# Optimization experiments

Hardware: AMD Instinct MI355X
Metric: run time of the kernel (lower is better)

Reference implementation:

```python
import jax, jax.numpy as jnp
import numpy as np

T, S, B, D, H, DH, DI = 1024, 1024, 4, 1024, 16, 64, 4096
SCALE = 1.0 / (DH ** 0.5)


def _ln(x, g, b, eps=1e-5):
    m = jnp.mean(x, axis=-1, keepdims=True)
    v = jnp.mean((x - m) ** 2, axis=-1, keepdims=True)
    return (x - m) * jax.lax.rsqrt(v + eps) * g + b


def setup_inputs() -> dict:
    key = jax.random.key(0)
    ks = jax.random.split(key, 16)
    s = 0.02
    inp = {
        "dec_inp": jax.random.normal(ks[0], (T, B, D), jnp.float32),
        "enc_out": jax.random.normal(ks[1], (T, B, D), jnp.float32),
        # causal mask for self-attn: [qlen, klen, bsz], True = masked
        "dec_mask": jnp.broadcast_to(jnp.triu(jnp.ones((T, T), bool), 1)[:, :, None], (T, T, B)),
        # encoder padding mask: [klen, bsz], last 128 positions padded
        "enc_mask": jnp.broadcast_to((jnp.arange(S) >= S - 128)[:, None], (S, B)),
        # self-attn params
        "W_q1": jax.random.normal(ks[2], (D, H * DH), jnp.float32) * s,
        "W_kv1": jax.random.normal(ks[3], (D, 2 * H * DH), jnp.float32) * s,
        "W_o1": jax.random.normal(ks[4], (H * DH, D), jnp.float32) * s,
        "g1": jnp.ones((D,), jnp.float32), "b1": jnp.zeros((D,), jnp.float32),
        # cross-attn params
        "W_q2": jax.random.normal(ks[5], (D, H * DH), jnp.float32) * s,
        "W_kv2": jax.random.normal(ks[6], (D, 2 * H * DH), jnp.float32) * s,
        "W_o2": jax.random.normal(ks[7], (H * DH, D), jnp.float32) * s,
        "g2": jnp.ones((D,), jnp.float32), "b2": jnp.zeros((D,), jnp.float32),
        # FFN params
        "W_ff1": jax.random.normal(ks[8], (D, DI), jnp.float32) * s,
        "b_ff1": jnp.zeros((DI,), jnp.float32),
        "W_ff2": jax.random.normal(ks[9], (DI, D), jnp.float32) * s,
        "b_ff2": jnp.zeros((D,), jnp.float32),
        "g3": jnp.ones((D,), jnp.float32), "b3": jnp.zeros((D,), jnp.float32),
    }
    return inp


def reference(dec_inp, enc_out, dec_mask, enc_mask,
              W_q1, W_kv1, W_o1, g1, b1,
              W_q2, W_kv2, W_o2, g2, b2,
              W_ff1, b_ff1, W_ff2, b_ff2, g3, b3):
    # ---- self-attention (MultiHeadAttn, pre_lnorm=True, mems=None) ----
    # NOTE: q is computed from the UN-normalized h; k,v from LN(c) — faithful to source.
    c = _ln(dec_inp, g1, b1)
    q = (dec_inp @ W_q1).reshape(T, B, H, DH)
    kv = (c @ W_kv1)
    k, v = jnp.split(kv, 2, axis=-1)
    k = k.reshape(T, B, H, DH)
    v = v.reshape(T, B, H, DH)
    score = jnp.einsum('ibnd,jbnd->ijbn', q, k) * SCALE  # [T,T,B,H]
    score = jnp.where(dec_mask[:, :, :, None], -jnp.inf, score)
    prob = jax.nn.softmax(score, axis=1)
    vec = jnp.einsum('ijbn,jbnd->ibnd', prob, v).reshape(T, B, H * DH)
    out1 = dec_inp + vec @ W_o1

    # ---- cross-attention (ContextMultiHeadAttn, pre_lnorm=True) ----
    # NOTE: residual uses the layer-normed h (source reassigns h = layer_norm(h)).
    h2 = _ln(out1, g2, b2)
    q2 = (h2 @ W_q2).reshape(T, B, H, DH)
    kv2 = enc_out @ W_kv2  # enc_out is NOT layer-normed in source
    k2, v2 = jnp.split(kv2, 2, axis=-1)
    k2 = k2.reshape(S, B, H, DH)
    v2 = v2.reshape(S, B, H, DH)
    score2 = jnp.einsum('ibnd,jbnd->ijbn', q2, k2) * SCALE  # [T,S,B,H]
    score2 = jnp.where(enc_mask[None, :, :, None], -10000.0, score2)
    prob2 = jax.nn.softmax(score2, axis=1)
    vec2 = jnp.einsum('ijbn,jbnd->ibnd', prob2, v2).reshape(T, B, H * DH)
    out2 = h2 + vec2 @ W_o2

    # ---- position-wise FFN (pre_lnorm) ----
    h3 = _ln(out2, g3, b3)
    core = jax.nn.gelu(h3 @ W_ff1 + b_ff1, approximate=False) @ W_ff2 + b_ff2
    return out2 + core
```

## Files before the change

kernel.cpp:

```cpp
#include <hip/hip_runtime.h>
#include <hip/hip_bf16.h>

#define T_ 1024
#define S_ 1024
#define B_ 4
#define D_ 1024
#define H_ 16
#define DH_ 64
#define DI_ 4096
#define NTOK 4096

typedef __attribute__((ext_vector_type(8))) short bf16x8;
typedef __attribute__((ext_vector_type(4))) float f32x4;

__device__ __forceinline__ short f2bf(float f) {
  unsigned u = __builtin_bit_cast(unsigned, f);
  u += 0x7fffu + ((u >> 16) & 1u);
  return (short)(u >> 16);
}

__device__ __forceinline__ void g2l16(const void* g, void* l) {
  __builtin_amdgcn_global_load_lds(
      (const __attribute__((address_space(1))) unsigned int*)g,
      (__attribute__((address_space(3))) unsigned int*)l, 16, 0, 0);
}

__device__ __forceinline__ void bar() {
  asm volatile("" ::: "memory");
  __builtin_amdgcn_s_barrier();
  asm volatile("" ::: "memory");
}

template <int EPI>
__global__ __launch_bounds__(512, 2) void gemm8p(
    const short* __restrict__ A, const short* __restrict__ Bt,
    float* __restrict__ outF, short* __restrict__ outB,
    const float* __restrict__ res, const float* __restrict__ bias,
    int M, int N, int K) {
  __shared__ short sA[2][256 * 64];
  __shared__ short sB[2][256 * 64];
  const int tid = threadIdx.x;
  const int lane = tid & 63;
  const int w = tid >> 6;
  const int wm = w >> 2, wn = w & 3;
  const int r15 = lane & 15, g4 = lane >> 4;
  const size_t row0 = (size_t)blockIdx.x * 256;
  const size_t col0 = (size_t)blockIdx.y * 256;

  f32x4 acc[8][4];
#pragma unroll
  for (int i = 0; i < 8; i++)
#pragma unroll
    for (int j = 0; j < 4; j++) acc[i][j] = (f32x4){0.f, 0.f, 0.f, 0.f};

  auto stageA = [&](int buf, int s, int kt) {
    const int k0 = kt << 6;
#pragma unroll
    for (int j = 0; j < 2; ++j) {
      const int c = j * 8 + w;
      const int rb = ((c >> 3) << 7) + (s << 6) + ((c & 7) << 3);
      const int row = rb + (lane >> 3);
      const int col = k0 + (((lane & 7) ^ (row & 7)) << 3);
      g2l16(A + (row0 + row) * (size_t)K + col, &sA[buf][rb * 64]);
    }
  };
  auto stageB = [&](int buf, int s, int kt) {
    const int k0 = kt << 6;
#pragma unroll
    for (int j = 0; j < 2; ++j) {
      const int c = j * 8 + w;
      const int rb = ((c >> 2) << 6) + (s << 5) + ((c & 3) << 3);
      const int row = rb + (lane >> 3);
      const int col = k0 + (((lane & 7) ^ (row & 7)) << 3);
      g2l16(Bt + (col0 + row) * (size_t)K + col, &sB[buf][rb * 64]);
    }
  };

  const int nk = K >> 6;
  stageA(0, 0, 0); stageA(0, 1, 0); stageB(0, 0, 0); stageB(0, 1, 0);
  if (nk > 1) {
    stageA(1, 0, 1); stageB(1, 1, 1);
    asm volatile("s_waitcnt vmcnt(4)" ::: "memory");
  } else {
    asm volatile("s_waitcnt vmcnt(0)" ::: "memory");
  }
  bar();

  bf16x8 af[4][2], bv[2][2];
  for (int t = 0; t < nk; ++t) {
    const int cur = t & 1;
    const short* cA = sA[cur];
    const short* cB = sB[cur];
#pragma unroll
    for (int mi = 0; mi < 4; mi++) {
      const int rowA = wm * 128 + mi * 16 + r15;
#pragma unroll
      for (int kk = 0; kk < 2; kk++)
        af[mi][kk] = *(const bf16x8*)(cA + rowA * 64 +
                                      (((kk * 4 + g4) ^ (rowA & 7)) << 3));
    }
#pragma unroll
    for (int ni = 0; ni < 2; ni++) {
      const int rowB = wn * 64 + ni * 16 + r15;
#pragma unroll
      for (int kk = 0; kk < 2; kk++)
        bv[ni][kk] = *(const bf16x8*)(cB + rowB * 64 +
                                      (((kk * 4 + g4) ^ (rowB & 7)) << 3));
    }
    if (t + 1 < nk) stageA(cur ^ 1, 1, t + 1);
    bar();
    asm volatile("s_waitcnt lgkmcnt(0)" ::: "memory");
    __builtin_amdgcn_s_setprio(1);
#pragma unroll
    for (int kk = 0; kk < 2; kk++)
#pragma unroll
      for (int mi = 0; mi < 4; mi++)
#pragma unroll
        for (int ni = 0; ni < 2; ni++)
          acc[mi][ni] = __builtin_amdgcn_mfma_f32_16x16x32_bf16(
              af[mi][kk], bv[ni][kk], acc[mi][ni], 0, 0, 0);
    __builtin_amdgcn_s_setprio(0);
    bar();
#pragma unroll
    for (int ni = 0; ni < 2; ni++) {
      const int rowB = wn * 64 + (2 + ni) * 16 + r15;
#pragma unroll
      for (int kk = 0; kk < 2; kk++)
        bv[ni][kk] = *(const bf16x8*)(cB + rowB * 64 +
                                      (((kk * 4 + g4) ^ (rowB & 7)) << 3));
    }
    if (t + 1 < nk) stageB(cur ^ 1, 0, t + 1);
    bar();
    asm volatile("s_waitcnt lgkmcnt(0)" ::: "memory");
    __builtin_amdgcn_s_setprio(1);
#pragma unroll
    for (int kk = 0; kk < 2; kk++)
#pragma unroll
      for (int mi = 0; mi < 4; mi++)
#pragma unroll
        for (int ni = 0; ni < 2; ni++)
          acc[mi][2 + ni] = __builtin_amdgcn_mfma_f32_16x16x32_bf16(
              af[mi][kk], bv[ni][kk], acc[mi][2 + ni], 0, 0, 0);
    __builtin_amdgcn_s_setprio(0);
    bar();
#pragma unroll
    for (int mi = 0; mi < 4; mi++) {
      const int rowA = wm * 128 + (4 + mi) * 16 + r15;
#pragma unroll
      for (int kk = 0; kk < 2; kk++)
        af[mi][kk] = *(const bf16x8*)(cA + rowA * 64 +
                                      (((kk * 4 + g4) ^ (rowA & 7)) << 3));
    }
    if (t + 2 < nk) stageA(cur, 0, t + 2);
    bar();
    asm volatile("s_waitcnt lgkmcnt(0)" ::: "memory");
    __builtin_amdgcn_s_setprio(1);
#pragma unroll
    for (int kk = 0; kk < 2; kk++)
#pragma unroll
      for (int mi = 0; mi < 4; mi++)
#pragma unroll
        for (int ni = 0; ni < 2; ni++)
          acc[4 + mi][2 + ni] = __builtin_amdgcn_mfma_f32_16x16x32_bf16(
              af[mi][kk], bv[ni][kk], acc[4 + mi][2 + ni], 0, 0, 0);
    __builtin_amdgcn_s_setprio(0);
    bar();
#pragma unroll
    for (int ni = 0; ni < 2; ni++) {
      const int rowB = wn * 64 + ni * 16 + r15;
#pragma unroll
      for (int kk = 0; kk < 2; kk++)
        bv[ni][kk] = *(const bf16x8*)(cB + rowB * 64 +
                                      (((kk * 4 + g4) ^ (rowB & 7)) << 3));
    }
    if (t + 2 < nk) stageB(cur, 1, t + 2);
    bar();
    asm volatile("s_waitcnt lgkmcnt(0)" ::: "memory");
    __builtin_amdgcn_s_setprio(1);
#pragma unroll
    for (int kk = 0; kk < 2; kk++)
#pragma unroll
      for (int mi = 0; mi < 4; mi++)
#pragma unroll
        for (int ni = 0; ni < 2; ni++)
          acc[4 + mi][ni] = __builtin_amdgcn_mfma_f32_16x16x32_bf16(
              af[mi][kk], bv[ni][kk], acc[4 + mi][ni], 0, 0, 0);
    __builtin_amdgcn_s_setprio(0);
    if (t + 2 < nk)
      asm volatile("s_waitcnt vmcnt(4)" ::: "memory");
    else if (t + 1 < nk)
      asm volatile("s_waitcnt vmcnt(0)" ::: "memory");
    bar();
  }

#pragma unroll
  for (int mi = 0; mi < 8; mi++) {
    size_t row = row0 + wm * 128 + mi * 16 + (g4 << 2);
#pragma unroll
    for (int ni = 0; ni < 4; ni++) {
      size_t col = col0 + wn * 64 + ni * 16 + r15;
      float bcol = (EPI == 2 || EPI == 3) ? bias[col] : 0.f;
#pragma unroll
      for (int r = 0; r < 4; r++) {
        size_t idx = (row + r) * (size_t)N + col;
        float v = acc[mi][ni][r];
        if (EPI == 0) {
          outB[idx] = f2bf(v);
        } else if (EPI == 1) {
          outF[idx] = v + res[idx];
        } else if (EPI == 2) {
          float x = v + bcol;
          float gl = 0.5f * x * (1.f + erff(x * 0.70710678118654752f));
          outB[idx] = f2bf(gl);
        } else {
          outF[idx] = v + bcol + res[idx];
        }
      }
    }
  }
}

template <int EPI, int BN>
__global__ __launch_bounds__(256, 2) void gemm_bt(
    const short* __restrict__ A, const short* __restrict__ Bt,
    float* __restrict__ outF, short* __restrict__ outB,
    const float* __restrict__ res, const float* __restrict__ bias,
    short* __restrict__ Kgp, short* __restrict__ Vgp,
    int M, int N, int K) {
  constexpr int WCOLS = BN / 64;
  constexpr int MI = (WCOLS == 2) ? 4 : 2;
  constexpr int BLOADS = BN / 32;
  __shared__ short sA[2][128 * 64];
  __shared__ short sB[2][BN * 64];
  const int tid = threadIdx.x;
  const int lane = tid & 63;
  const int w = tid >> 6;
  const int wr = (WCOLS == 2) ? (w >> 1) : w;
  const int wc = (WCOLS == 2) ? (w & 1) : 0;
  const int r15 = lane & 15, g4 = lane >> 4;
  const size_t row0 = (size_t)blockIdx.x * 128;
  const size_t col0 = (size_t)blockIdx.y * BN;

  f32x4 acc[MI][4];
#pragma unroll
  for (int i = 0; i < MI; i++)
#pragma unroll
    for (int j = 0; j < 4; j++) acc[i][j] = (f32x4){0.f, 0.f, 0.f, 0.f};

  auto stage = [&](int buf, int kt) {
    const int k0 = kt << 6;
#pragma unroll
    for (int i = 0; i < 4; i++) {
      int flat = i * 256 + tid;
      int row = flat >> 3;
      int col = k0 + (((flat & 7) ^ (row & 7)) << 3);
      g2l16(A + (row0 + row) * (size_t)K + col, &sA[buf][(i * 256 + w * 64) * 8]);
    }
#pragma unroll
    for (int i = 0; i < BLOADS; i++) {
      int flat = i * 256 + tid;
      int row = flat >> 3;
      int col = k0 + (((flat & 7) ^ (row & 7)) << 3);
      g2l16(Bt + (col0 + row) * (size_t)K + col, &sB[buf][(i * 256 + w * 64) * 8]);
    }
  };

  stage(0, 0);
  __syncthreads();

  const int nk = K >> 6;
  for (int kt = 0; kt < nk; ++kt) {
    const int cur = kt & 1;
    if (kt + 1 < nk) stage(cur ^ 1, kt + 1);
#pragma unroll
    for (int kk = 0; kk < 2; ++kk) {
      bf16x8 af[MI], bfr[4];
#pragma unroll
      for (int mi = 0; mi < MI; mi++) {
        int rowA = wr * (MI * 16) + mi * 16 + r15;
        af[mi] = *(const bf16x8*)(&sA[cur][rowA * 64 +
                                           (((kk * 4 + g4) ^ (rowA & 7)) << 3)]);
      }
#pragma unroll
      for (int ni = 0; ni < 4; ni++) {
        int rowB = wc * 64 + ni * 16 + r15;
        bfr[ni] = *(const bf16x8*)(&sB[cur][rowB * 64 +
                                            (((kk * 4 + g4) ^ (rowB & 7)) << 3)]);
      }
#pragma unroll
      for (int mi = 0; mi < MI; mi++)
#pragma unroll
        for (int ni = 0; ni < 4; ni++)
          acc[mi][ni] = __builtin_amdgcn_mfma_f32_16x16x32_bf16(af[mi], bfr[ni],
                                                                acc[mi][ni], 0, 0, 0);
    }
    __syncthreads();
  }

#pragma unroll
  for (int mi = 0; mi < MI; mi++) {
    size_t row = row0 + wr * (MI * 16) + mi * 16 + (g4 << 2);
#pragma unroll
    for (int ni = 0; ni < 4; ni++) {
      size_t col = col0 + wc * 64 + ni * 16 + r15;
      float bcol = (EPI == 2 || EPI == 3) ? bias[col] : 0.f;
#pragma unroll
      for (int r = 0; r < 4; r++) {
        size_t idx = (row + r) * (size_t)N + col;
        float v = acc[mi][ni][r];
        if (EPI == 0) {
          outB[idx] = f2bf(v);
        } else if (EPI == 1) {
          outF[idx] = v + res[idx];
        } else if (EPI == 2) {
          float x = v + bcol;
          float gl = 0.5f * x * (1.f + erff(x * 0.70710678118654752f));
          outB[idx] = f2bf(gl);
        } else if (EPI == 3) {
          outF[idx] = v + bcol + res[idx];
        } else {
          int tt = (int)(row + r) >> 2;
          int bb = (int)(row + r) & 3;
          int cc = (int)col;
          if (cc < 1024) {
            int hh = cc >> 6, dd = cc & 63;
            size_t base = (size_t)(bb * 16 + hh) * 65536 + (size_t)tt * 64;
            Kgp[base + ((((dd >> 3) ^ (tt & 7)) << 3) | (dd & 7))] = f2bf(v * 0.125f);
          } else {
            int hh = (cc >> 6) - 16, dd = cc & 63;
            size_t base = (size_t)(bb * 16 + hh) * 65536 + (size_t)(tt >> 6) * 4096;
            Vgp[base + ((tt >> 3) & 7) * 512 + dd * 8 + (tt & 7)] = f2bf(v);
          }
        }
      }
    }
  }
}

template <int MODE>
__global__ __launch_bounds__(256, 2) void attn_k2(const short* __restrict__ Qm,
                                                  const short* __restrict__ Kg,
                                                  const short* __restrict__ Vg,
                                                  short* __restrict__ Om) {
  __shared__ short Kl[2][4096];
  __shared__ short Vl[2][4096];
  __shared__ short Pl[4][2048];
  const int tid = threadIdx.x;
  const int lane = tid & 63;
  const int w = tid >> 6;
  const int r15 = lane & 15, g4 = lane >> 4;
  const int bh = blockIdx.x;
  const int qt = blockIdx.y;
  const int b = bh >> 4, h = bh & 15;
  const int qbase = qt * 128 + w * 32;
  const int ktDiag = qbase >> 6;

  bf16x8 qf[2][2];
#pragma unroll
  for (int g = 0; g < 2; g++)
#pragma unroll
    for (int hf = 0; hf < 2; hf++) {
      int row = qbase + g * 16 + r15;
      qf[g][hf] = *(const bf16x8*)(Qm + ((size_t)(row * 4 + b)) * 1024 + h * 64 +
                                   hf * 32 + g4 * 8);
    }

  const size_t kvbase = (size_t)bh * 65536;
  const int nkt = (MODE == 0) ? (2 * qt + 2) : 14;

  f32x4 o[2][4];
#pragma unroll
  for (int g = 0; g < 2; g++)
#pragma unroll
    for (int ni = 0; ni < 4; ni++) o[g][ni] = (f32x4){0.f, 0.f, 0.f, 0.f};
  float mrun[2][4], lrun[2][4];
#pragma unroll
  for (int g = 0; g < 2; g++)
#pragma unroll
    for (int r = 0; r < 4; r++) { mrun[g][r] = -1e30f; lrun[g][r] = 0.f; }

  {
    const size_t tb = kvbase;
#pragma unroll
    for (int i = 0; i < 2; i++) {
      g2l16(Kg + tb + (size_t)(i * 256 + tid) * 8, &Kl[0][(i * 256 + w * 64) * 8]);
      g2l16(Vg + tb + (size_t)(i * 256 + tid) * 8, &Vl[0][(i * 256 + w * 64) * 8]);
    }
  }
  __syncthreads();

  for (int kt = 0; kt < nkt; kt++) {
    const int cur = kt & 1;
    if (kt + 1 < nkt) {
      const size_t tb = kvbase + (size_t)(kt + 1) * 4096;
#pragma unroll
      for (int i = 0; i < 2; i++) {
        g2l16(Kg + tb + (size_t)(i * 256 + tid) * 8,
              &Kl[cur ^ 1][(i * 256 + w * 64) * 8]);
        g2l16(Vg + tb + (size_t)(i * 256 + tid) * 8,
              &Vl[cur ^ 1][(i * 256 + w * 64) * 8]);
      }
    }

    const bool active = (MODE == 1) || (kt * 64 <= qbase + 31);
    if (active) {
      bf16x8 kb[4][2];
#pragma unroll
      for (int ni = 0; ni < 4; ni++) {
        int row = ni * 16 + r15;
        kb[ni][0] = *(const bf16x8*)(&Kl[cur][row * 64 + ((g4 ^ (row & 7)) << 3)]);
        kb[ni][1] =
            *(const bf16x8*)(&Kl[cur][row * 64 + (((g4 + 4) ^ (row & 7)) << 3)]);
      }
      f32x4 sf[2][4];
#pragma unroll
      for (int g = 0; g < 2; g++)
#pragma unroll
        for (int ni = 0; ni < 4; ni++) {
          f32x4 s = (f32x4){0.f, 0.f, 0.f, 0.f};
          s = __builtin_amdgcn_mfma_f32_16x16x32_bf16(qf[g][0], kb[ni][0], s, 0, 0, 0);
          s = __builtin_amdgcn_mfma_f32_16x16x32_bf16(qf[g][1], kb[ni][1], s, 0, 0, 0);
          sf[g][ni] = s;
        }
      if (MODE == 0 && kt >= ktDiag) {
#pragma unroll
        for (int g = 0; g < 2; g++)
#pragma unroll
          for (int ni = 0; ni < 4; ni++)
#pragma unroll
            for (int r = 0; r < 4; r++) {
              int q = qbase + g * 16 + g4 * 4 + r;
              int key = kt * 64 + ni * 16 + r15;
              if (key > q) sf[g][ni][r] = -1e30f;
            }
      }
#pragma unroll
      for (int g = 0; g < 2; g++) {
        float corr[4];
#pragma unroll
        for (int r = 0; r < 4; r++) {
          float m = fmaxf(fmaxf(sf[g][0][r], sf[g][1][r]),
                          fmaxf(sf[g][2][r], sf[g][3][r]));
          m = fmaxf(m, __shfl_xor(m, 1));
          m = fmaxf(m, __shfl_xor(m, 2));
          m = fmaxf(m, __shfl_xor(m, 4));
          m = fmaxf(m, __shfl_xor(m, 8));
          float mn = fmaxf(mrun[g][r], m);
          corr[r] = __expf(mrun[g][r] - mn);
          mrun[g][r] = mn;
        }
        float rs[4] = {0.f, 0.f, 0.f, 0.f};
#pragma unroll
        for (int ni = 0; ni < 4; ni++)
#pragma unroll
          for (int r = 0; r < 4; r++) {
            float p = __expf(sf[g][ni][r] - mrun[g][r]);
            sf[g][ni][r] = p;
            rs[r] += p;
          }
#pragma unroll
        for (int r = 0; r < 4; r++) {
          rs[r] += __shfl_xor(rs[r], 1);
          rs[r] += __shfl_xor(rs[r], 2);
          rs[r] += __shfl_xor(rs[r], 4);
          rs[r] += __shfl_xor(rs[r], 8);
          lrun[g][r] = lrun[g][r] * corr[r] + rs[r];
        }
#pragma unroll
        for (int ni = 0; ni < 4; ni++)
#pragma unroll
          for (int r = 0; r < 4; r++) o[g][ni][r] *= corr[r];
#pragma unroll
        for (int ni = 0; ni < 4; ni++)
#pragma unroll
          for (int r = 0; r < 4; r++) {
            int qr = g * 16 + g4 * 4 + r;
            int key = ni * 16 + r15;
            Pl[w][qr * 64 + ((((key >> 3) ^ ((qr >> 1) & 7)) << 3) | (key & 7))] =
                f2bf(sf[g][ni][r]);
          }
      }
#pragma unroll
      for (int kk = 0; kk < 2; kk++) {
        int gw = kk * 4 + g4;
        bf16x8 pa0 = *(const bf16x8*)(&Pl[w][r15 * 64 + ((gw ^ ((r15 >> 1) & 7)) << 3)]);
        bf16x8 pa1 =
            *(const bf16x8*)(&Pl[w][(16 + r15) * 64 + ((gw ^ ((r15 >> 1) & 7)) << 3)]);
#pragma unroll
        for (int ni = 0; ni < 4; ni++) {
          bf16x8 vb = *(const bf16x8*)(&Vl[cur][(gw * 64 + ni * 16 + r15) * 8]);
          o[0][ni] = __builtin_amdgcn_mfma_f32_16x16x32_bf16(pa0, vb, o[0][ni], 0, 0, 0);
          o[1][ni] = __builtin_amdgcn_mfma_f32_16x16x32_bf16(pa1, vb, o[1][ni], 0, 0, 0);
        }
      }
    }
    __syncthreads();
  }

#pragma unroll
  for (int g = 0; g < 2; g++) {
    float inv[4];
#pragma unroll
    for (int r = 0; r < 4; r++) inv[r] = 1.f / lrun[g][r];
#pragma unroll
    for (int ni = 0; ni < 4; ni++) {
      int col = h * 64 + ni * 16 + r15;
#pragma unroll
      for (int r = 0; r < 4; r++) {
        int tg = qbase + g * 16 + g4 * 4 + r;
        Om[((size_t)(tg * 4 + b)) * 1024 + col] = f2bf(o[g][ni][r] * inv[r]);
      }
    }
  }
}

__global__ __launch_bounds__(256) void ln_k(const float* __restrict__ x,
                                            const float* __restrict__ gw,
                                            const float* __restrict__ bw,
                                            float* __restrict__ outF,
                                            short* __restrict__ outB,
                                            short* __restrict__ outXB) {
  const int row = blockIdx.x, tid = threadIdx.x;
  const float4 v = ((const float4*)(x + (size_t)row * 1024))[tid];
  float s = v.x + v.y + v.z + v.w;
  float ss = v.x * v.x + v.y * v.y + v.z * v.z + v.w * v.w;
#pragma unroll
  for (int d = 32; d >= 1; d >>= 1) {
    s += __shfl_xor(s, d);
    ss += __shfl_xor(ss, d);
  }
  __shared__ float red[8];
  const int w = tid >> 6;
  if ((tid & 63) == 0) { red[w] = s; red[4 + w] = ss; }
  __syncthreads();
  s = red[0] + red[1] + red[2] + red[3];
  ss = red[4] + red[5] + red[6] + red[7];
  const float mean = s * (1.f / 1024.f);
  const float var = ss * (1.f / 1024.f) - mean * mean;
  const float rstd = rsqrtf(var + 1e-5f);
  const float4 gv = ((const float4*)gw)[tid];
  const float4 bv = ((const float4*)bw)[tid];
  float4 y;
  y.x = (v.x - mean) * rstd * gv.x + bv.x;
  y.y = (v.y - mean) * rstd * gv.y + bv.y;
  y.z = (v.z - mean) * rstd * gv.z + bv.z;
  y.w = (v.w - mean) * rstd * gv.w + bv.w;
  if (outF) ((float4*)(outF + (size_t)row * 1024))[tid] = y;
  if (outB) {
    short4 ob;
    ob.x = f2bf(y.x); ob.y = f2bf(y.y); ob.z = f2bf(y.z); ob.w = f2bf(y.w);
    ((short4*)(outB + (size_t)row * 1024))[tid] = ob;
  }
  if (outXB) {
    short4 ob;
    ob.x = f2bf(v.x); ob.y = f2bf(v.y); ob.z = f2bf(v.z); ob.w = f2bf(v.w);
    ((short4*)(outXB + (size_t)row * 1024))[tid] = ob;
  }
}

__global__ __launch_bounds__(256) void cvt_bf16(const float* __restrict__ in,
                                                short* __restrict__ out) {
  const size_t i = (size_t)blockIdx.x * 256 + threadIdx.x;
  const float4 v = ((const float4*)in)[i];
  short4 ob;
  ob.x = f2bf(v.x); ob.y = f2bf(v.y); ob.z = f2bf(v.z); ob.w = f2bf(v.w);
  ((short4*)out)[i] = ob;
}

__global__ __launch_bounds__(256) void tr_cvt(const float* __restrict__ in,
                                              short* __restrict__ out, int K, int N) {
  __shared__ float t[64][65];
  const int tid = threadIdx.x;
  const int k0 = blockIdx.x * 64, n0 = blockIdx.y * 64;
#pragma unroll
  for (int i = 0; i < 16; i++) {
    int flat = i * 256 + tid;
    int r = flat >> 6, c = flat & 63;
    t[r][c] = in[(size_t)(k0 + r) * N + n0 + c];
  }
  __syncthreads();
#pragma unroll
  for (int i = 0; i < 16; i++) {
    int flat = i * 256 + tid;
    int r = flat >> 6, c = flat & 63;
    out[(size_t)(n0 + r) * K + k0 + c] = f2bf(t[c][r]);
  }
}

extern "C" void kernel_launch(void* const* d_in, const int* in_sizes, int n_in,
                              void* d_out, int out_size, void* d_ws, size_t ws_size,
                              hipStream_t stream) {
  const float* dec_inp = (const float*)d_in[0];
  const float* enc_out = (const float*)d_in[1];
  const float* W_q1 = (const float*)d_in[4];
  const float* W_kv1 = (const float*)d_in[5];
  const float* W_o1 = (const float*)d_in[6];
  const float* g1 = (const float*)d_in[7];
  const float* b1 = (const float*)d_in[8];
  const float* W_q2 = (const float*)d_in[9];
  const float* W_kv2 = (const float*)d_in[10];
  const float* W_o2 = (const float*)d_in[11];
  const float* g2 = (const float*)d_in[12];
  const float* b2 = (const float*)d_in[13];
  const float* W_ff1 = (const float*)d_in[14];
  const float* b_ff1 = (const float*)d_in[15];
  const float* W_ff2 = (const float*)d_in[16];
  const float* b_ff2 = (const float*)d_in[17];
  const float* g3 = (const float*)d_in[18];
  const float* b3 = (const float*)d_in[19];
  float* out = (float*)d_out;

  char* ws = (char*)d_ws;
  size_t off = 0;
  auto alloc = [&](size_t bytes) -> void* {
    void* p = ws + off;
    off += (bytes + 255) & ~(size_t)255;
    return p;
  };
  short* Wq1t = (short*)alloc(1024ull * 1024 * 2);
  short* Wkv1t = (short*)alloc(2048ull * 1024 * 2);
  short* Wo1t = (short*)alloc(1024ull * 1024 * 2);
  short* Wq2t = (short*)alloc(1024ull * 1024 * 2);
  short* Wkv2t = (short*)alloc(2048ull * 1024 * 2);
  short* Wo2t = (short*)alloc(1024ull * 1024 * 2);
  short* Wff1t = (short*)alloc(4096ull * 1024 * 2);
  short* Wff2t = (short*)alloc(1024ull * 4096 * 2);
  short* Xbf = (short*)alloc((size_t)NTOK * 1024 * 2);
  short* Ebf = (short*)alloc((size_t)NTOK * 1024 * 2);
  short* Cbf = (short*)alloc((size_t)NTOK * 1024 * 2);
  short* Qb = (short*)alloc((size_t)NTOK * 1024 * 2);
  short* Kg = (short*)alloc(64ull * 65536 * 2);
  short* Vg = (short*)alloc(64ull * 65536 * 2);
  short* VECb = (short*)alloc((size_t)NTOK * 1024 * 2);
  float* OUT1 = (float*)alloc((size_t)NTOK * 1024 * 4);
  float* H2f = (float*)alloc((size_t)NTOK * 1024 * 4);
  float* OUT2 = (float*)alloc((size_t)NTOK * 1024 * 4);
  short* FF1 = (short*)alloc((size_t)NTOK * 4096 * 2);
  short* H2b = Xbf;
  short* H3b = Cbf;

  dim3 blk(256, 1, 1);

  tr_cvt<<<dim3(16, 16), blk, 0, stream>>>(W_q1, Wq1t, 1024, 1024);
  tr_cvt<<<dim3(16, 32), blk, 0, stream>>>(W_kv1, Wkv1t, 1024, 2048);
  tr_cvt<<<dim3(16, 16), blk, 0, stream>>>(W_o1, Wo1t, 1024, 1024);
  tr_cvt<<<dim3(16, 16), blk, 0, stream>>>(W_q2, Wq2t, 1024, 1024);
  tr_cvt<<<dim3(16, 32), blk, 0, stream>>>(W_kv2, Wkv2t, 1024, 2048);
  tr_cvt<<<dim3(16, 16), blk, 0, stream>>>(W_o2, Wo2t, 1024, 1024);
  tr_cvt<<<dim3(16, 64), blk, 0, stream>>>(W_ff1, Wff1t, 1024, 4096);
  tr_cvt<<<dim3(64, 16), blk, 0, stream>>>(W_ff2, Wff2t, 4096, 1024);

  cvt_bf16<<<4096, blk, 0, stream>>>(enc_out, Ebf);
  ln_k<<<4096, blk, 0, stream>>>(dec_inp, g1, b1, nullptr, Cbf, Xbf);

  gemm_bt<0, 64><<<dim3(32, 16), blk, 0, stream>>>(
      Xbf, Wq1t, nullptr, Qb, nullptr, nullptr, nullptr, nullptr, 4096, 1024, 1024);
  gemm_bt<4, 128><<<dim3(32, 16), blk, 0, stream>>>(
      Cbf, Wkv1t, nullptr, nullptr, nullptr, nullptr, Kg, Vg, 4096, 2048, 1024);
  attn_k2<0><<<dim3(64, 8), blk, 0, stream>>>(Qb, Kg, Vg, VECb);
  gemm_bt<1, 64><<<dim3(32, 16), blk, 0, stream>>>(
      VECb, Wo1t, OUT1, nullptr, dec_inp, nullptr, nullptr, nullptr, 4096, 1024, 1024);
  ln_k<<<4096, blk, 0, stream>>>(OUT1, g2, b2, H2f, H2b, nullptr);
  gemm_bt<0, 64><<<dim3(32, 16), blk, 0, stream>>>(
      H2b, Wq2t, nullptr, Qb, nullptr, nullptr, nullptr, nullptr, 4096, 1024, 1024);
  gemm_bt<4, 128><<<dim3(32, 16), blk, 0, stream>>>(
      Ebf, Wkv2t, nullptr, nullptr, nullptr, nullptr, Kg, Vg, 4096, 2048, 1024);
  attn_k2<1><<<dim3(64, 8), blk, 0, stream>>>(Qb, Kg, Vg, VECb);
  gemm_bt<1, 64><<<dim3(32, 16), blk, 0, stream>>>(
      VECb, Wo2t, OUT2, nullptr, H2f, nullptr, nullptr, nullptr, 4096, 1024, 1024);
  ln_k<<<4096, blk, 0, stream>>>(OUT2, g3, b3, nullptr, H3b, nullptr);
  gemm8p<2><<<dim3(16, 16), dim3(512, 1, 1), 0, stream>>>(
      H3b, Wff1t, nullptr, FF1, nullptr, b_ff1, 4096, 4096, 1024);
  gemm_bt<3, 64><<<dim3(32, 16), blk, 0, stream>>>(
      FF1, Wff2t, out, nullptr, OUT2, b_ff2, nullptr, nullptr, 4096, 1024, 4096);
}
```

Before: 382.5 us.

## Swizzle GEMM blocks across XCDs, permute V keys, vectorize P stores

Adds an XCD-aware remap of block indices in both GEMM kernels so neighbouring tiles land on the same chiplet and share L2. Permutes the key order inside each 64-key V tile so every lane can write its four softmax probabilities as one packed short4 LDS store instead of sixteen scalar stores, and adjusts the P swizzle to match. Raises the attention kernel's occupancy hint from 2 to 3 blocks per SM, which may add register pressure. The V permutation and the P layout must stay consistent for results to be correct.

```diff
diff --git a/kernel.cpp b/kernel.cpp
--- a/kernel.cpp
+++ b/kernel.cpp
@@ -29,6 +29,15 @@
   asm volatile("" ::: "memory");
   __builtin_amdgcn_s_barrier();
   asm volatile("" ::: "memory");
+}
+
+__device__ __forceinline__ void xcd_swz(int& bx, int& by) {
+  const int gx = gridDim.x;
+  const int id0 = blockIdx.y * gx + blockIdx.x;
+  const int cpx = (gx * gridDim.y) >> 3;
+  const int nid = (id0 & 7) * cpx + (id0 >> 3);
+  bx = nid % gx;
+  by = nid / gx;
 }
 
 template <int EPI>
@@ -44,8 +53,10 @@
   const int w = tid >> 6;
   const int wm = w >> 2, wn = w & 3;
   const int r15 = lane & 15, g4 = lane >> 4;
-  const size_t row0 = (size_t)blockIdx.x * 256;
-  const size_t col0 = (size_t)blockIdx.y * 256;
+  int bx, by;
+  xcd_swz(bx, by);
+  const size_t row0 = (size_t)bx * 256;
+  const size_t col0 = (size_t)by * 256;
 
   f32x4 acc[8][4];
 #pragma unroll
@@ -238,8 +249,10 @@
   const int wr = (WCOLS == 2) ? (w >> 1) : w;
   const int wc = (WCOLS == 2) ? (w & 1) : 0;
   const int r15 = lane & 15, g4 = lane >> 4;
-  const size_t row0 = (size_t)blockIdx.x * 128;
-  const size_t col0 = (size_t)blockIdx.y * BN;
+  int bx, by;
+  xcd_swz(bx, by);
+  const size_t row0 = (size_t)bx * 128;
+  const size_t col0 = (size_t)by * BN;
 
   f32x4 acc[MI][4];
 #pragma unroll
@@ -328,8 +341,10 @@
             Kgp[base + ((((dd >> 3) ^ (tt & 7)) << 3) | (dd & 7))] = f2bf(v * 0.125f);
           } else {
             int hh = (cc >> 6) - 16, dd = cc & 63;
+            int k6 = tt & 63;
+            int kap = ((k6 & 15) << 2) | (k6 >> 4);
             size_t base = (size_t)(bb * 16 + hh) * 65536 + (size_t)(tt >> 6) * 4096;
-            Vgp[base + ((tt >> 3) & 7) * 512 + dd * 8 + (tt & 7)] = f2bf(v);
+            Vgp[base + (kap >> 3) * 512 + dd * 8 + (kap & 7)] = f2bf(v);
           }
         }
       }
@@ -338,7 +353,7 @@
 }
 
 template <int MODE>
-__global__ __launch_bounds__(256, 2) void attn_k2(const short* __restrict__ Qm,
+__global__ __launch_bounds__(256, 3) void attn_k2(const short* __restrict__ Qm,
                                                   const short* __restrict__ Kg,
                                                   const short* __restrict__ Vg,
                                                   short* __restrict__ Om) {
@@ -471,21 +486,23 @@
 #pragma unroll
           for (int r = 0; r < 4; r++) o[g][ni][r] *= corr[r];
 #pragma unroll
-        for (int ni = 0; ni < 4; ni++)
-#pragma unroll
-          for (int r = 0; r < 4; r++) {
-            int qr = g * 16 + g4 * 4 + r;
-            int key = ni * 16 + r15;
-            Pl[w][qr * 64 + ((((key >> 3) ^ ((qr >> 1) & 7)) << 3) | (key & 7))] =
-                f2bf(sf[g][ni][r]);
-          }
+        for (int r = 0; r < 4; r++) {
+          int qr = g * 16 + g4 * 4 + r;
+          short4 pk;
+          pk.x = f2bf(sf[g][0][r]);
+          pk.y = f2bf(sf[g][1][r]);
+          pk.z = f2bf(sf[g][2][r]);
+          pk.w = f2bf(sf[g][3][r]);
+          int gran = (r15 >> 1) ^ (qr & 7);
+          *(short4*)(&Pl[w][qr * 64 + gran * 8 + (r15 & 1) * 4]) = pk;
+        }
       }
 #pragma unroll
       for (int kk = 0; kk < 2; kk++) {
         int gw = kk * 4 + g4;
-        bf16x8 pa0 = *(const bf16x8*)(&Pl[w][r15 * 64 + ((gw ^ ((r15 >> 1) & 7)) << 3)]);
+        bf16x8 pa0 = *(const bf16x8*)(&Pl[w][r15 * 64 + ((gw ^ (r15 & 7)) << 3)]);
         bf16x8 pa1 =
-            *(const bf16x8*)(&Pl[w][(16 + r15) * 64 + ((gw ^ ((r15 >> 1) & 7)) << 3)]);
+            *(const bf16x8*)(&Pl[w][(16 + r15) * 64 + ((gw ^ (r15 & 7)) << 3)]);
 #pragma unroll
         for (int ni = 0; ni < 4; ni++) {
           bf16x8 vb = *(const bf16x8*)(&Vl[cur][(gw * 64 + ni * 16 + r15) * 8]);
```

Result: slower. 399.3 us (+4.4%).
